# Kernel tuning notes

Hardware: AMD Instinct MI355X
Metric: run time of the kernel (lower is better)

The kernel has to match this reference:

```python
import jax, jax.numpy as jnp
import numpy as np

B, S, D = 2, 2048, 4096
H, HD = 32, 128  # n_heads, head_dim
P = 30           # prefix_len
ROPE_THETA = 10000.0


def _rope_tables():
    inv = 1.0 / (ROPE_THETA ** (np.arange(0, HD, 2, dtype=np.float64) / HD))
    f = np.outer(np.arange(S, dtype=np.float64), inv)  # [S, HD/2]
    return jnp.asarray(np.cos(f), jnp.float32), jnp.asarray(np.sin(f), jnp.float32)


def setup_inputs() -> dict:
    key = jax.random.key(0)
    ks = jax.random.split(key, 7)
    scale = 0.02
    x = jax.random.normal(ks[0], (B, S, D), jnp.float32)
    freqs_cos, freqs_sin = _rope_tables()
    prefix = jax.random.normal(ks[1], (1, P, D), jnp.float32) * scale
    prefix_gate = jax.random.normal(ks[2], (H,), jnp.float32) * 0.1
    wq = jax.random.normal(ks[3], (D, H * HD), jnp.float32) * scale
    wk = jax.random.normal(ks[4], (D, H * HD), jnp.float32) * scale
    wv = jax.random.normal(ks[5], (D, H * HD), jnp.float32) * scale
    wo = jax.random.normal(ks[6], (H * HD, D), jnp.float32) * scale
    return dict(x=x, freqs_cos=freqs_cos, freqs_sin=freqs_sin, prefix=prefix,
                prefix_gate=prefix_gate, wq=wq, wk=wk, wv=wv, wo=wo, start_pos=0)


def _apply_rope(t, cos, sin):
    # t: [b, s, h, hd]; cos/sin: [s, hd/2] -> broadcast [1, s, 1, hd/2]
    tr = t.reshape(*t.shape[:-1], HD // 2, 2)
    t0, t1 = tr[..., 0], tr[..., 1]
    c = cos[None, :, None, :]
    s = sin[None, :, None, :]
    o0 = t0 * c - t1 * s
    o1 = t0 * s + t1 * c
    return jnp.stack([o0, o1], axis=-1).reshape(t.shape)


def _attend(q, k, v, causal):
    # q: [b, sq, h, d]; k, v: [b, sk, h, d]
    scale = 1.0 / jnp.sqrt(jnp.asarray(HD, q.dtype))
    scores = jnp.einsum('bqhd,bkhd->bhqk', q, k) * scale
    if causal:
        sq, sk = q.shape[1], k.shape[1]
        mask = jnp.tril(jnp.ones((sq, sk), bool))
        scores = jnp.where(mask[None, None], scores, jnp.asarray(-1e30, scores.dtype))
    probs = jax.nn.softmax(scores, axis=-1)
    return jnp.einsum('bhqk,bkhd->bqhd', probs, v)


def reference(x, freqs_cos, freqs_sin, prefix, prefix_gate, wq, wk, wv, wo, start_pos):
    bsz, seqlen, _ = x.shape
    xq = (x @ wq).reshape(bsz, seqlen, H, HD)
    xk = (x @ wk).reshape(bsz, seqlen, H, HD)
    xv = (x @ wv).reshape(bsz, seqlen, H, HD)
    xq = _apply_rope(xq, freqs_cos, freqs_sin)
    xk = _apply_rope(xk, freqs_cos, freqs_sin)
    # n_rep == 1 (MHA), repeat_kv is identity
    out = _attend(xq, xk, xv, causal=True)  # [b, s, h, hd]
    # prefix-tuning branch: no RoPE on prefix k/v, non-causal attention
    pk = jnp.broadcast_to(prefix @ wk, (bsz, P, H * HD)).reshape(bsz, P, H, HD)
    pv = jnp.broadcast_to(prefix @ wv, (bsz, P, H * HD)).reshape(bsz, P, H, HD)
    prefix_delta = _attend(xq, pk, pv, causal=False)
    gate = jnp.tanh(prefix_gate).reshape(1, 1, H, 1)
    out = out + gate * prefix_delta
    out = out.reshape(bsz, seqlen, H * HD)
    return out @ wo
```

## Files before the change

kernel.cpp:

```cpp
#include <hip/hip_runtime.h>
#include <hip/hip_bf16.h>

#define AS1 __attribute__((address_space(1)))
#define AS3 __attribute__((address_space(3)))

typedef __attribute__((ext_vector_type(8))) short bf16x8;
typedef __attribute__((ext_vector_type(4))) float f32x4;

#define B_ 2
#define S_ 2048
#define D_ 4096
#define H_ 32
#define HD_ 128
#define P_ 30

__device__ __forceinline__ short f2b(float f) {
  union { __hip_bfloat16 h; short s; } u;
  u.h = __float2bfloat16(f);
  return u.s;
}
__device__ __forceinline__ float b2f(short s) {
  union { short s; __hip_bfloat16 h; } u;
  u.s = s;
  return __bfloat162float(u.h);
}
__device__ __forceinline__ void gload16(const void* g, void* l) {
  __builtin_amdgcn_global_load_lds((const AS1 void*)g, (AS3 void*)l, 16, 0, 0);
}

__global__ __launch_bounds__(256) void convert_f32_bf16(const float* __restrict__ in,
                                                        short* __restrict__ out) {
  size_t i = ((size_t)blockIdx.x * 256 + threadIdx.x) * 4;
  float4 v = *reinterpret_cast<const float4*>(in + i);
  short4 o;
  o.x = f2b(v.x); o.y = f2b(v.y); o.z = f2b(v.z); o.w = f2b(v.w);
  *reinterpret_cast<short4*>(out + i) = o;
}

__global__ __launch_bounds__(256) void pad_prefix(const float* __restrict__ p,
                                                  short* __restrict__ pb) {
  int i = blockIdx.x * 256 + threadIdx.x;
  int row = i >> 12, col = i & 4095;
  pb[i] = (row < P_) ? f2b(p[row * D_ + col]) : (short)0;
}

__global__ void transpose_convert(const float* __restrict__ W, short* __restrict__ Wt,
                                  int K, int N) {
  __shared__ float t[32][33];
  int bx = blockIdx.x, by = blockIdx.y;
  int tx = threadIdx.x, ty = threadIdx.y;
#pragma unroll
  for (int i = 0; i < 4; ++i) {
    int r = ty * 4 + i;
    t[r][tx] = W[(size_t)(by * 32 + r) * N + bx * 32 + tx];
  }
  __syncthreads();
#pragma unroll
  for (int i = 0; i < 4; ++i) {
    int r = ty * 4 + i;
    Wt[(size_t)(bx * 32 + r) * K + by * 32 + tx] = f2b(t[tx][r]);
  }
}

__global__ __launch_bounds__(256) void rope_kernel(short* __restrict__ t,
                                                   const float* __restrict__ fc,
                                                   const float* __restrict__ fs) {
  size_t g = ((size_t)blockIdx.x * 256 + threadIdx.x) * 8;
  int d = (int)(g & 127);
  int s = (int)((g >> 12) & 2047);
  bf16x8 v = *reinterpret_cast<bf16x8*>(t + g);
  int i0 = d >> 1;
  float4 c = *reinterpret_cast<const float4*>(fc + (size_t)s * 64 + i0);
  float4 sn = *reinterpret_cast<const float4*>(fs + (size_t)s * 64 + i0);
  float cc[4] = {c.x, c.y, c.z, c.w};
  float ss[4] = {sn.x, sn.y, sn.z, sn.w};
  bf16x8 o;
#pragma unroll
  for (int p = 0; p < 4; ++p) {
    float t0 = b2f(v[2 * p]), t1 = b2f(v[2 * p + 1]);
    o[2 * p] = f2b(t0 * cc[p] - t1 * ss[p]);
    o[2 * p + 1] = f2b(t0 * ss[p] + t1 * cc[p]);
  }
  *reinterpret_cast<bf16x8*>(t + g) = o;
}

template <int OM>
__global__ __launch_bounds__(256) void gemm_bt(const short* __restrict__ A,
                                               const short* __restrict__ Bt,
                                               void* __restrict__ Cv,
                                               int M, int N, int K) {
  __shared__ short As[128 * 32];
  __shared__ short Bs[128 * 32];
  const int tid = threadIdx.x;
  const int lane = tid & 63;
  const int wbase = tid & 192;
  const int wr = ((tid >> 7) & 1) * 64;
  const int wc = ((tid >> 6) & 1) * 64;
  const int lr = lane & 15;
  const int lk = (lane >> 4) * 8;
  int lin = blockIdx.y * gridDim.x + blockIdx.x;
  int nwg = gridDim.x * gridDim.y;
  int cpx = nwg >> 3;
  int swz = (lin & 7) * cpx + (lin >> 3);
  const int bm = swz / gridDim.x, bn = swz % gridDim.x;
  f32x4 acc[4][4] = {};
  const short* Ab = A + (size_t)bm * 128 * K;
  const short* Bb = Bt + (size_t)bn * 128 * K;
  for (int kt = 0; kt < K; kt += 32) {
    __syncthreads();
#pragma unroll
    for (int i = 0; i < 2; ++i) {
      int f = i * 256 + tid;
      int row = f >> 2, col = (f & 3) * 8;
      gload16(Ab + (size_t)row * K + kt + col, &As[(i * 256 + wbase) * 8]);
      gload16(Bb + (size_t)row * K + kt + col, &Bs[(i * 256 + wbase) * 8]);
    }
    __syncthreads();
    bf16x8 af[4], bfr[4];
#pragma unroll
    for (int m = 0; m < 4; ++m)
      af[m] = *reinterpret_cast<const bf16x8*>(&As[(wr + m * 16 + lr) * 32 + lk]);
#pragma unroll
    for (int n = 0; n < 4; ++n)
      bfr[n] = *reinterpret_cast<const bf16x8*>(&Bs[(wc + n * 16 + lr) * 32 + lk]);
#pragma unroll
    for (int m = 0; m < 4; ++m)
#pragma unroll
      for (int n = 0; n < 4; ++n)
        acc[m][n] = __builtin_amdgcn_mfma_f32_16x16x32_bf16(af[m], bfr[n], acc[m][n], 0, 0, 0);
  }
  const int row0 = bm * 128 + wr + (lane >> 4) * 4;
  const int col0 = bn * 128 + wc + lr;
  if constexpr (OM == 3) {
    short* C = (short*)Cv;
#pragma unroll
    for (int m = 0; m < 4; ++m)
#pragma unroll
      for (int n = 0; n < 4; ++n) {
        short4 pk;
        pk.x = f2b(acc[m][n][0]); pk.y = f2b(acc[m][n][1]);
        pk.z = f2b(acc[m][n][2]); pk.w = f2b(acc[m][n][3]);
        size_t idx = (size_t)(col0 + n * 16) * M + row0 + m * 16;
        *reinterpret_cast<short4*>(&C[idx]) = pk;
      }
  } else {
#pragma unroll
    for (int m = 0; m < 4; ++m)
#pragma unroll
      for (int n = 0; n < 4; ++n)
#pragma unroll
        for (int j = 0; j < 4; ++j) {
          size_t idx = (size_t)(row0 + m * 16 + j) * N + col0 + n * 16;
          ((short*)Cv)[idx] = f2b(acc[m][n][j]);
        }
  }
}

#define PHASE(mh, kh, STAGE, TAIL)                                              \
  {                                                                             \
    bf16x8 af[4], bfr[4];                                                       \
    const int pg = (((kh)*4 + lg) ^ (lr & 7)) * 8;                              \
    _Pragma("unroll") for (int mm = 0; mm < 4; ++mm)                            \
      af[mm] = *(const bf16x8*)&As[slot][(wr + (mh)*64 + mm*16 + lr)*64 + pg];  \
    _Pragma("unroll") for (int nn = 0; nn < 4; ++nn)                            \
      bfr[nn] = *(const bf16x8*)&Bs[slot][(wc + nn*16 + lr)*64 + pg];           \
    STAGE;                                                                      \
    __builtin_amdgcn_s_barrier();                                               \
    asm volatile("s_waitcnt lgkmcnt(0)" ::: "memory");                          \
    __builtin_amdgcn_sched_barrier(0);                                          \
    __builtin_amdgcn_s_setprio(1);                                              \
    _Pragma("unroll") for (int mm = 0; mm < 4; ++mm)                            \
      _Pragma("unroll") for (int nn = 0; nn < 4; ++nn)                          \
        acc[(mh)*4 + mm][nn] = __builtin_amdgcn_mfma_f32_16x16x32_bf16(         \
            af[mm], bfr[nn], acc[(mh)*4 + mm][nn], 0, 0, 0);                    \
    __builtin_amdgcn_s_setprio(0);                                              \
    TAIL;                                                                       \
    __builtin_amdgcn_s_barrier();                                               \
  }

template <int OM>
__global__ __launch_bounds__(512, 2) void gemm256(const short* __restrict__ A,
                                                  const short* __restrict__ Bt,
                                                  void* __restrict__ Cv,
                                                  int M, int N, int K) {
  __shared__ short As[2][256 * 64];
  __shared__ short Bs[2][256 * 64];
  const int tid = threadIdx.x;
  const int w = tid >> 6;
  const int lane = tid & 63;
  const int lr = lane & 15, lg = lane >> 4;
  const int wr = (w >> 2) * 128;
  const int wc = (w & 3) * 64;
  int lin = blockIdx.y * gridDim.x + blockIdx.x;
  int nwg = gridDim.x * gridDim.y;
  int cpx = nwg >> 3;
  int swz = (lin & 7) * cpx + (lin >> 3);
  const int bm = swz / gridDim.x, bn = swz % gridDim.x;

  const short* Ab = A + (size_t)bm * 256 * K;
  const short* Bb = Bt + (size_t)bn * 256 * K;
  const int NT = K >> 6;

  f32x4 acc[8][4] = {};

  auto stA = [&](int slot_, int r0, int kt) {
    int row = r0 + (lane >> 3);
    int gsrc = (lane & 7) ^ ((lane >> 3) & 7);
    gload16(Ab + (size_t)row * K + kt + gsrc * 8, &As[slot_][r0 * 64]);
  };
  auto stB = [&](int slot_, int r0, int kt) {
    int row = r0 + (lane >> 3);
    int gsrc = (lane & 7) ^ ((lane >> 3) & 7);
    gload16(Bb + (size_t)row * K + kt + gsrc * 8, &Bs[slot_][r0 * 64]);
  };

  const int q2 = w * 2, q4 = w * 4;
  const int rt0 = (q2 < 8 ? 0 : 64) + q2 * 8;
  const int rt1 = (q2 + 1 < 8 ? 0 : 64) + (q2 + 1) * 8;

  {
#pragma unroll
    for (int i = 0; i < 4; ++i) stB(0, (q4 + i) * 8, 0);
    stA(0, rt0, 0); stA(0, 64 + rt0, 0);
    stA(0, rt1, 0); stA(0, 64 + rt1, 0);
#pragma unroll
    for (int i = 0; i < 4; ++i) stB(1, (q4 + i) * 8, 64);
    stA(1, rt0, 64); stA(1, 64 + rt0, 64);
    stA(1, rt1, 64); stA(1, 64 + rt1, 64);
  }
  asm volatile("s_waitcnt vmcnt(8)" ::: "memory");
  __builtin_amdgcn_s_barrier();

  for (int t = 0; t < NT; ++t) {
    const int slot = t & 1;
    const int ns = slot ^ 1;
    const int kt1 = (t + 1) << 6, kt2 = (t + 2) << 6;
    const bool s6 = (t >= 1) && (t + 1 < NT);
    const bool s2 = (t + 2 < NT);

    PHASE(0, 0,
          { if (s6) { stB(ns, (q4 + 0) * 8, kt1); stB(ns, (q4 + 1) * 8, kt1); } },
          {});
    PHASE(0, 1,
          { if (s6) { stB(ns, (q4 + 2) * 8, kt1); stB(ns, (q4 + 3) * 8, kt1);
                      stA(ns, 64 + rt0, kt1);     stA(ns, 64 + rt1, kt1); } },
          {});
    PHASE(1, 0,
          { if (s2) stA(slot, rt0, kt2); },
          {});
    PHASE(1, 1,
          { if (s2) stA(slot, rt1, kt2); },
          { if (s2) asm volatile("s_waitcnt vmcnt(2)" ::: "memory");
            else    asm volatile("s_waitcnt vmcnt(0)" ::: "memory"); });
  }

  const int row0 = bm * 256 + wr + lg * 4;
  const int col0 = bn * 256 + wc + lr;
  if constexpr (OM == 2) {
    short* C = (short*)Cv;
#pragma unroll
    for (int mf = 0; mf < 8; ++mf)
#pragma unroll
      for (int n = 0; n < 4; ++n) {
        int r0 = row0 + mf * 16;
        int bb = r0 >> 11, s0 = r0 & 2047;
        short4 pk;
        pk.x = f2b(acc[mf][n][0]); pk.y = f2b(acc[mf][n][1]);
        pk.z = f2b(acc[mf][n][2]); pk.w = f2b(acc[mf][n][3]);
        size_t idx = ((size_t)(bb * 4096 + col0 + n * 16)) * 2048 + s0;
        *reinterpret_cast<short4*>(&C[idx]) = pk;
      }
  } else {
#pragma unroll
    for (int mf = 0; mf < 8; ++mf)
#pragma unroll
      for (int n = 0; n < 4; ++n)
#pragma unroll
        for (int j = 0; j < 4; ++j) {
          size_t idx = (size_t)(row0 + mf * 16 + j) * N + col0 + n * 16;
          if constexpr (OM == 1) ((short*)Cv)[idx] = f2b(acc[mf][n][j]);
          else ((float*)Cv)[idx] = acc[mf][n][j];
        }
  }
}

__global__ __launch_bounds__(1024, 4) void attn_kernel(
    const short* __restrict__ qb, const short* __restrict__ kb, const short* __restrict__ vt,
    const short* __restrict__ pkb, const short* __restrict__ pvt,
    const float* __restrict__ gate, short* __restrict__ ab) {
  __shared__ short Ks[2][64 * 128];
  __shared__ short Vs[128 * 64];
  __shared__ short Ps[16][16 * 64];
  const int tid = threadIdx.x;
  const int wave = tid >> 6, lane = tid & 63;
  const int lr = lane & 15, lg = lane >> 4;
  const int lin = blockIdx.x;
  const int qt = 7 - (lin >> 6);
  const int bh = lin & 63;
  const int b = bh >> 5, h = bh & 31;

  bf16x8 aq[4];
  {
    const short* qrow = qb + ((size_t)(b * S_ + qt * 256 + wave * 16 + lr) * H_ + h) * HD_;
#pragma unroll
    for (int kk = 0; kk < 4; ++kk)
      aq[kk] = *reinterpret_cast<const bf16x8*>(qrow + kk * 32 + lg * 8);
  }

  float m = -1e30f, l = 0.f, l2 = 0.f;
  f32x4 o[8] = {}, o2[8] = {};

  const short* kb_bh = kb + ((size_t)b * S_ * H_ + h) * HD_;
  const short* vt_bh = vt + ((size_t)(b * H_ + h)) * HD_ * S_;

  auto stageK = [&](int t, int buf) {
    int row = tid >> 4;
    int col = ((tid & 15) ^ (row & 7)) * 8;
    gload16(kb_bh + (size_t)(t * 64 + row) * (H_ * HD_) + col,
            &Ks[buf][(tid & 960) * 8]);
  };
  auto stagePK = [&](int buf) {
    int row = tid >> 4;
    int col = ((tid & 15) ^ (row & 7)) * 8;
    gload16(pkb + (size_t)row * 4096 + h * HD_ + col, &Ks[buf][(tid & 960) * 8]);
  };
  auto loadV = [&](int t, bf16x8& vr) {
    int row = tid >> 3;
    vr = *reinterpret_cast<const bf16x8*>(vt_bh + (size_t)row * S_ + t * 64 + (tid & 7) * 8);
  };
  auto loadPV = [&](bf16x8& vr) {
    int row = tid >> 3;
    vr = *reinterpret_cast<const bf16x8*>(pvt + ((size_t)h * HD_ + row) * 128 + (tid & 7) * 8);
  };
  auto writeV = [&](const bf16x8& vr) {
    int row = tid >> 3;
    int gran = (tid & 7) ^ (row & 7);
    *reinterpret_cast<bf16x8*>(&Vs[row * 64 + gran * 8]) = vr;
  };

  const float scale = 0.08838834764831845f;

  auto qkt = [&](int buf, f32x4 sc[4]) {
    __builtin_amdgcn_s_setprio(1);
#pragma unroll
    for (int cb = 0; cb < 4; ++cb) {
      int tok = cb * 16 + lr;
#pragma unroll
      for (int kk = 0; kk < 4; ++kk) {
        int addr = tok * 128 + (((kk * 4 + lg) ^ (tok & 7)) * 8);
        bf16x8 bk = *reinterpret_cast<const bf16x8*>(&Ks[buf][addr]);
        sc[cb] = __builtin_amdgcn_mfma_f32_16x16x32_bf16(bk, aq[kk], sc[cb], 0, 0, 0);
      }
    }
    __builtin_amdgcn_s_setprio(0);
  };
  auto pv = [&](f32x4* acc_) {
#pragma unroll
    for (int kk = 0; kk < 2; ++kk) {
      bf16x8 ap = *reinterpret_cast<const bf16x8*>(
          &Ps[wave][lr * 64 + (((kk * 4 + lg) ^ (lr & 7)) * 8)]);
      __builtin_amdgcn_s_setprio(1);
#pragma unroll
      for (int nb = 0; nb < 8; ++nb) {
        int d = nb * 16 + lr;
        bf16x8 bv = *reinterpret_cast<const bf16x8*>(
            &Vs[d * 64 + (((kk * 4 + lg) ^ (lr & 7)) * 8)]);
        acc_[nb] = __builtin_amdgcn_mfma_f32_16x16x32_bf16(ap, bv, acc_[nb], 0, 0, 0);
      }
      __builtin_amdgcn_s_setprio(0);
    }
  };

  auto process = [&](int t, bool diag) {
    const int buf = t & 1;
    f32x4 sc[4] = {};
    qkt(buf, sc);
    const int rowg = qt * 256 + wave * 16 + lr;
#pragma unroll
    for (int cb = 0; cb < 4; ++cb)
#pragma unroll
      for (int j = 0; j < 4; ++j) {
        int colg = t * 64 + cb * 16 + lg * 4 + j;
        float v = sc[cb][j] * scale;
        sc[cb][j] = (!diag || colg <= rowg) ? v : -1e30f;
      }
    float mx = sc[0][0];
#pragma unroll
    for (int cb = 0; cb < 4; ++cb)
#pragma unroll
      for (int j = 0; j < 4; ++j) mx = fmaxf(mx, sc[cb][j]);
    mx = fmaxf(mx, __shfl_xor(mx, 16));
    mx = fmaxf(mx, __shfl_xor(mx, 32));
    float mn = fmaxf(m, mx);
    float alpha = __expf(m - mn);
    m = mn;
    float rs = 0.f;
#pragma unroll
    for (int cb = 0; cb < 4; ++cb) {
      short4 pk;
      float p0 = __expf(sc[cb][0] - mn);
      float p1 = __expf(sc[cb][1] - mn);
      float p2 = __expf(sc[cb][2] - mn);
      float p3 = __expf(sc[cb][3] - mn);
      rs += (p0 + p1) + (p2 + p3);
      pk.x = f2b(p0); pk.y = f2b(p1); pk.z = f2b(p2); pk.w = f2b(p3);
      int gran = (cb * 2 + (lg >> 1)) ^ (lr & 7);
      *reinterpret_cast<short4*>(&Ps[wave][lr * 64 + gran * 8 + (lg & 1) * 4]) = pk;
    }
    rs += __shfl_xor(rs, 16);
    rs += __shfl_xor(rs, 32);
    l = l * alpha + rs;
    f32x4 av;
#pragma unroll
    for (int j = 0; j < 4; ++j) av[j] = __shfl(alpha, lg * 4 + j);
#pragma unroll
    for (int nb = 0; nb < 8; ++nb)
#pragma unroll
      for (int j = 0; j < 4; ++j) o[nb][j] *= av[j];
    pv(o);
  };

  auto processPrefix = [&]() {
    f32x4 sc[4] = {};
    qkt(0, sc);
#pragma unroll
    for (int cb = 0; cb < 4; ++cb)
#pragma unroll
      for (int j = 0; j < 4; ++j) {
        int coll = cb * 16 + lg * 4 + j;
        float v = sc[cb][j] * scale;
        sc[cb][j] = (coll < P_) ? v : -1e30f;
      }
    float mx = sc[0][0];
#pragma unroll
    for (int cb = 0; cb < 4; ++cb)
#pragma unroll
      for (int j = 0; j < 4; ++j) mx = fmaxf(mx, sc[cb][j]);
    mx = fmaxf(mx, __shfl_xor(mx, 16));
    mx = fmaxf(mx, __shfl_xor(mx, 32));
    float rs = 0.f;
#pragma unroll
    for (int cb = 0; cb < 4; ++cb) {
      short4 pk;
      float p0 = __expf(sc[cb][0] - mx);
      float p1 = __expf(sc[cb][1] - mx);
      float p2 = __expf(sc[cb][2] - mx);
      float p3 = __expf(sc[cb][3] - mx);
      rs += (p0 + p1) + (p2 + p3);
      pk.x = f2b(p0); pk.y = f2b(p1); pk.z = f2b(p2); pk.w = f2b(p3);
      int gran = (cb * 2 + (lg >> 1)) ^ (lr & 7);
      *reinterpret_cast<short4*>(&Ps[wave][lr * 64 + gran * 8 + (lg & 1) * 4]) = pk;
    }
    rs += __shfl_xor(rs, 16);
    rs += __shfl_xor(rs, 32);
    l2 = rs;
    pv(o2);
  };

  const int nt = 4 * (qt + 1);
  bf16x8 vr;

  stagePK(0);
  loadPV(vr);
  __syncthreads();
  writeV(vr);
  __syncthreads();
  processPrefix();
  __syncthreads();

  stageK(0, 0);
  loadV(0, vr);
  __syncthreads();
  writeV(vr);
  __syncthreads();
  for (int t = 0; t < nt; ++t) {
    const bool more = (t + 1 < nt);
    if (more) {
      loadV(t + 1, vr);
      stageK(t + 1, (t + 1) & 1);
    }
    process(t, t >= 4 * qt);
    __syncthreads();
    if (more) writeV(vr);
    __syncthreads();
  }

  {
    float g = tanhf(gate[h]);
    f32x4 lv, lv2;
#pragma unroll
    for (int j = 0; j < 4; ++j) {
      lv[j] = __shfl(l, lg * 4 + j);
      lv2[j] = __shfl(l2, lg * 4 + j);
    }
#pragma unroll
    for (int j = 0; j < 4; ++j) {
      int q = qt * 256 + wave * 16 + lg * 4 + j;
      float inv = 1.f / lv[j];
      float inv2 = g / lv2[j];
      size_t base = ((size_t)(b * S_ + q) * H_ + h) * HD_;
#pragma unroll
      for (int nb = 0; nb < 8; ++nb)
        ab[base + nb * 16 + lr] = f2b(o[nb][j] * inv + o2[nb][j] * inv2);
    }
  }
}

extern "C" void kernel_launch(void* const* d_in, const int* in_sizes, int n_in,
                              void* d_out, int out_size, void* d_ws, size_t ws_size,
                              hipStream_t stream) {
  const float* x = (const float*)d_in[0];
  const float* fc = (const float*)d_in[1];
  const float* fs = (const float*)d_in[2];
  const float* prefix = (const float*)d_in[3];
  const float* gate = (const float*)d_in[4];
  const float* wq = (const float*)d_in[5];
  const float* wk = (const float*)d_in[6];
  const float* wv = (const float*)d_in[7];
  const float* wo = (const float*)d_in[8];
  float* out = (float*)d_out;

  char* ws = (char*)d_ws;
  const size_t SZ = (size_t)4096 * 4096 * 2;
  short* xb = (short*)(ws);
  short* wT = (short*)(ws + SZ);
  short* qbuf = (short*)(ws + 2 * SZ);
  short* kbuf = (short*)(ws + 3 * SZ);
  short* vT = (short*)(ws + 4 * SZ);
  short* pb = (short*)(ws + 5 * SZ);
  short* pkb = (short*)(ws + 5 * SZ + (1 << 20));
  short* pvt = (short*)(ws + 5 * SZ + (2 << 20));
  short* abuf = xb;

  dim3 tcg(128, 128), tcb(32, 8);
  dim3 gg(16, 16), gp(32, 1);

  convert_f32_bf16<<<16384, 256, 0, stream>>>(x, xb);
  pad_prefix<<<2048, 256, 0, stream>>>(prefix, pb);

  transpose_convert<<<tcg, tcb, 0, stream>>>(wq, wT, 4096, 4096);
  gemm256<1><<<gg, 512, 0, stream>>>(xb, wT, qbuf, 4096, 4096, 4096);

  transpose_convert<<<tcg, tcb, 0, stream>>>(wk, wT, 4096, 4096);
  gemm256<1><<<gg, 512, 0, stream>>>(xb, wT, kbuf, 4096, 4096, 4096);
  gemm_bt<1><<<gp, 256, 0, stream>>>(pb, wT, pkb, 128, 4096, 4096);

  transpose_convert<<<tcg, tcb, 0, stream>>>(wv, wT, 4096, 4096);
  gemm256<2><<<gg, 512, 0, stream>>>(xb, wT, vT, 4096, 4096, 4096);
  gemm_bt<3><<<gp, 256, 0, stream>>>(pb, wT, pvt, 128, 4096, 4096);

  rope_kernel<<<8192, 256, 0, stream>>>(qbuf, fc, fs);
  rope_kernel<<<8192, 256, 0, stream>>>(kbuf, fc, fs);

  attn_kernel<<<512, 1024, 0, stream>>>(qbuf, kbuf, vT, pkb, pvt, gate, abuf);

  transpose_convert<<<tcg, tcb, 0, stream>>>(wo, wT, 4096, 4096);
  gemm256<0><<<gg, 512, 0, stream>>>(abuf, wT, out, 4096, 4096, 4096);
}
```

Baseline: 915.9 us.

## Process 128-key tiles per attention iteration and merge RoPE launches

The attention loop now stages 128 keys (K and V) per iteration instead of 64. This halves the number of loop iterations, barrier pairs and online-softmax rescales, and runs two QK^T/PV halves back to back. LDS use grows to about 128KB per block and each thread holds extra score and probability registers, so register pressure may rise. Separately, the two RoPE launches for Q and K are merged into one grid with a y dimension.

```diff
diff --git a/kernel.cpp b/kernel.cpp
--- a/kernel.cpp
+++ b/kernel.cpp
@@ -62,9 +62,11 @@
   }
 }
 
-__global__ __launch_bounds__(256) void rope_kernel(short* __restrict__ t,
+__global__ __launch_bounds__(256) void rope_kernel(short* __restrict__ q,
+                                                   short* __restrict__ k,
                                                    const float* __restrict__ fc,
                                                    const float* __restrict__ fs) {
+  short* t = blockIdx.y ? k : q;
   size_t g = ((size_t)blockIdx.x * 256 + threadIdx.x) * 8;
   int d = (int)(g & 127);
   int s = (int)((g >> 12) & 2047);
@@ -288,8 +290,8 @@
     const short* __restrict__ qb, const short* __restrict__ kb, const short* __restrict__ vt,
     const short* __restrict__ pkb, const short* __restrict__ pvt,
     const float* __restrict__ gate, short* __restrict__ ab) {
-  __shared__ short Ks[2][64 * 128];
-  __shared__ short Vs[128 * 64];
+  __shared__ short Ks[2][128 * 128];
+  __shared__ short Vs[128 * 128];
   __shared__ short Ps[16][16 * 64];
   const int tid = threadIdx.x;
   const int wave = tid >> 6, lane = tid & 63;
@@ -313,38 +315,54 @@
   const short* kb_bh = kb + ((size_t)b * S_ * H_ + h) * HD_;
   const short* vt_bh = vt + ((size_t)(b * H_ + h)) * HD_ * S_;
 
-  auto stageK = [&](int t, int buf) {
+  auto stageK = [&](int r, int buf) {
+#pragma unroll
+    for (int c = 0; c < 2; ++c) {
+      int f = c * 1024 + tid;
+      int row = f >> 4;
+      int col = ((f & 15) ^ (row & 7)) * 8;
+      gload16(kb_bh + (size_t)(r * 128 + row) * (H_ * HD_) + col,
+              &Ks[buf][(c * 1024 + (tid & 960)) * 8]);
+    }
+  };
+  auto stagePK = [&]() {
     int row = tid >> 4;
     int col = ((tid & 15) ^ (row & 7)) * 8;
-    gload16(kb_bh + (size_t)(t * 64 + row) * (H_ * HD_) + col,
-            &Ks[buf][(tid & 960) * 8]);
-  };
-  auto stagePK = [&](int buf) {
-    int row = tid >> 4;
-    int col = ((tid & 15) ^ (row & 7)) * 8;
-    gload16(pkb + (size_t)row * 4096 + h * HD_ + col, &Ks[buf][(tid & 960) * 8]);
-  };
-  auto loadV = [&](int t, bf16x8& vr) {
-    int row = tid >> 3;
-    vr = *reinterpret_cast<const bf16x8*>(vt_bh + (size_t)row * S_ + t * 64 + (tid & 7) * 8);
+    gload16(pkb + (size_t)row * 4096 + h * HD_ + col, &Ks[0][(tid & 960) * 8]);
+  };
+  auto loadV = [&](int r, bf16x8 vr[2]) {
+#pragma unroll
+    for (int c = 0; c < 2; ++c) {
+      int f = c * 1024 + tid;
+      int d = f >> 4, g = f & 15;
+      vr[c] = *reinterpret_cast<const bf16x8*>(vt_bh + (size_t)d * S_ + r * 128 + g * 8);
+    }
+  };
+  auto writeV = [&](const bf16x8 vr[2]) {
+#pragma unroll
+    for (int c = 0; c < 2; ++c) {
+      int f = c * 1024 + tid;
+      int d = f >> 4, g = f & 15;
+      int gs = (g & 8) | ((g & 7) ^ (d & 7));
+      *reinterpret_cast<bf16x8*>(&Vs[d * 128 + gs * 8]) = vr[c];
+    }
   };
   auto loadPV = [&](bf16x8& vr) {
-    int row = tid >> 3;
-    vr = *reinterpret_cast<const bf16x8*>(pvt + ((size_t)h * HD_ + row) * 128 + (tid & 7) * 8);
-  };
-  auto writeV = [&](const bf16x8& vr) {
-    int row = tid >> 3;
-    int gran = (tid & 7) ^ (row & 7);
-    *reinterpret_cast<bf16x8*>(&Vs[row * 64 + gran * 8]) = vr;
+    int d = tid >> 3, g = tid & 7;
+    vr = *reinterpret_cast<const bf16x8*>(pvt + ((size_t)h * HD_ + d) * 128 + g * 8);
+  };
+  auto writePV = [&](const bf16x8& vr) {
+    int d = tid >> 3, g = tid & 7;
+    *reinterpret_cast<bf16x8*>(&Vs[d * 128 + ((g ^ (d & 7)) * 8)]) = vr;
   };
 
   const float scale = 0.08838834764831845f;
 
-  auto qkt = [&](int buf, f32x4 sc[4]) {
+  auto qkt = [&](int buf, int hh, f32x4 sc[4]) {
     __builtin_amdgcn_s_setprio(1);
 #pragma unroll
     for (int cb = 0; cb < 4; ++cb) {
-      int tok = cb * 16 + lr;
+      int tok = hh * 64 + cb * 16 + lr;
 #pragma unroll
       for (int kk = 0; kk < 4; ++kk) {
         int addr = tok * 128 + (((kk * 4 + lg) ^ (tok & 7)) * 8);
@@ -354,7 +372,7 @@
     }
     __builtin_amdgcn_s_setprio(0);
   };
-  auto pv = [&](f32x4* acc_) {
+  auto pv = [&](int hh, f32x4* acc_) {
 #pragma unroll
     for (int kk = 0; kk < 2; ++kk) {
       bf16x8 ap = *reinterpret_cast<const bf16x8*>(
@@ -364,48 +382,60 @@
       for (int nb = 0; nb < 8; ++nb) {
         int d = nb * 16 + lr;
         bf16x8 bv = *reinterpret_cast<const bf16x8*>(
-            &Vs[d * 64 + (((kk * 4 + lg) ^ (lr & 7)) * 8)]);
+            &Vs[d * 128 + ((hh * 8 + ((kk * 4 + lg) ^ (d & 7))) * 8)]);
         acc_[nb] = __builtin_amdgcn_mfma_f32_16x16x32_bf16(ap, bv, acc_[nb], 0, 0, 0);
       }
       __builtin_amdgcn_s_setprio(0);
     }
   };
 
-  auto process = [&](int t, bool diag) {
-    const int buf = t & 1;
-    f32x4 sc[4] = {};
-    qkt(buf, sc);
+  auto process = [&](int r, bool diag) {
+    const int buf = r & 1;
+    f32x4 sc[2][4] = {};
+    qkt(buf, 0, sc[0]);
+    qkt(buf, 1, sc[1]);
     const int rowg = qt * 256 + wave * 16 + lr;
 #pragma unroll
-    for (int cb = 0; cb < 4; ++cb)
-#pragma unroll
-      for (int j = 0; j < 4; ++j) {
-        int colg = t * 64 + cb * 16 + lg * 4 + j;
-        float v = sc[cb][j] * scale;
-        sc[cb][j] = (!diag || colg <= rowg) ? v : -1e30f;
-      }
-    float mx = sc[0][0];
-#pragma unroll
-    for (int cb = 0; cb < 4; ++cb)
-#pragma unroll
-      for (int j = 0; j < 4; ++j) mx = fmaxf(mx, sc[cb][j]);
+    for (int hh = 0; hh < 2; ++hh)
+#pragma unroll
+      for (int cb = 0; cb < 4; ++cb)
+#pragma unroll
+        for (int j = 0; j < 4; ++j) {
+          int colg = r * 128 + hh * 64 + cb * 16 + lg * 4 + j;
+          float v = sc[hh][cb][j] * scale;
+          sc[hh][cb][j] = (!diag || colg <= rowg) ? v : -1e30f;
+        }
+    float mx = sc[0][0][0];
+#pragma unroll
+    for (int hh = 0; hh < 2; ++hh)
+#pragma unroll
+      for (int cb = 0; cb < 4; ++cb)
+#pragma unroll
+        for (int j = 0; j < 4; ++j) mx = fmaxf(mx, sc[hh][cb][j]);
     mx = fmaxf(mx, __shfl_xor(mx, 16));
     mx = fmaxf(mx, __shfl_xor(mx, 32));
     float mn = fmaxf(m, mx);
     float alpha = __expf(m - mn);
     m = mn;
     float rs = 0.f;
+    short4 pk1[4];
 #pragma unroll
     for (int cb = 0; cb < 4; ++cb) {
       short4 pk;
-      float p0 = __expf(sc[cb][0] - mn);
-      float p1 = __expf(sc[cb][1] - mn);
-      float p2 = __expf(sc[cb][2] - mn);
-      float p3 = __expf(sc[cb][3] - mn);
+      float p0 = __expf(sc[0][cb][0] - mn);
+      float p1 = __expf(sc[0][cb][1] - mn);
+      float p2 = __expf(sc[0][cb][2] - mn);
+      float p3 = __expf(sc[0][cb][3] - mn);
       rs += (p0 + p1) + (p2 + p3);
       pk.x = f2b(p0); pk.y = f2b(p1); pk.z = f2b(p2); pk.w = f2b(p3);
       int gran = (cb * 2 + (lg >> 1)) ^ (lr & 7);
       *reinterpret_cast<short4*>(&Ps[wave][lr * 64 + gran * 8 + (lg & 1) * 4]) = pk;
+      float q0 = __expf(sc[1][cb][0] - mn);
+      float q1 = __expf(sc[1][cb][1] - mn);
+      float q2 = __expf(sc[1][cb][2] - mn);
+      float q3 = __expf(sc[1][cb][3] - mn);
+      rs += (q0 + q1) + (q2 + q3);
+      pk1[cb].x = f2b(q0); pk1[cb].y = f2b(q1); pk1[cb].z = f2b(q2); pk1[cb].w = f2b(q3);
     }
     rs += __shfl_xor(rs, 16);
     rs += __shfl_xor(rs, 32);
@@ -417,12 +447,18 @@
     for (int nb = 0; nb < 8; ++nb)
 #pragma unroll
       for (int j = 0; j < 4; ++j) o[nb][j] *= av[j];
-    pv(o);
+    pv(0, o);
+#pragma unroll
+    for (int cb = 0; cb < 4; ++cb) {
+      int gran = (cb * 2 + (lg >> 1)) ^ (lr & 7);
+      *reinterpret_cast<short4*>(&Ps[wave][lr * 64 + gran * 8 + (lg & 1) * 4]) = pk1[cb];
+    }
+    pv(1, o);
   };
 
   auto processPrefix = [&]() {
     f32x4 sc[4] = {};
-    qkt(0, sc);
+    qkt(0, 0, sc);
 #pragma unroll
     for (int cb = 0; cb < 4; ++cb)
 #pragma unroll
@@ -454,16 +490,19 @@
     rs += __shfl_xor(rs, 16);
     rs += __shfl_xor(rs, 32);
     l2 = rs;
-    pv(o2);
-  };
-
-  const int nt = 4 * (qt + 1);
-  bf16x8 vr;
-
-  stagePK(0);
-  loadPV(vr);
-  __syncthreads();
-  writeV(vr);
+    pv(0, o2);
+  };
+
+  const int nr = 2 * (qt + 1);
+  bf16x8 vr[2];
+
+  stagePK();
+  {
+    bf16x8 pvr;
+    loadPV(pvr);
+    __syncthreads();
+    writePV(pvr);
+  }
   __syncthreads();
   processPrefix();
   __syncthreads();
@@ -473,13 +512,13 @@
   __syncthreads();
   writeV(vr);
   __syncthreads();
-  for (int t = 0; t < nt; ++t) {
-    const bool more = (t + 1 < nt);
+  for (int r = 0; r < nr; ++r) {
+    const bool more = (r + 1 < nr);
     if (more) {
-      loadV(t + 1, vr);
-      stageK(t + 1, (t + 1) & 1);
-    }
-    process(t, t >= 4 * qt);
+      loadV(r + 1, vr);
+      stageK(r + 1, (r + 1) & 1);
+    }
+    process(r, r >= 2 * qt);
     __syncthreads();
     if (more) writeV(vr);
     __syncthreads();
@@ -549,8 +588,7 @@
   gemm256<2><<<gg, 512, 0, stream>>>(xb, wT, vT, 4096, 4096, 4096);
   gemm_bt<3><<<gp, 256, 0, stream>>>(pb, wT, pvt, 128, 4096, 4096);
 
-  rope_kernel<<<8192, 256, 0, stream>>>(qbuf, fc, fs);
-  rope_kernel<<<8192, 256, 0, stream>>>(kbuf, fc, fs);
+  rope_kernel<<<dim3(8192, 2), 256, 0, stream>>>(qbuf, kbuf, fc, fs);
 
   attn_kernel<<<512, 1024, 0, stream>>>(qbuf, kbuf, vT, pkb, pvt, gate, abuf);
 
```

New measurement: 924.7 us. About the same (+1.0%).
